# Performance work log

Hardware: AMD Instinct MI355X
Metric: run time of the kernel (lower is better)

## Reference

```python
import jax, jax.numpy as jnp
import numpy as np
import math

B, S, D = 16, 2048, 128
MASK_SENTINEL = -100

def setup_inputs() -> dict:
    key = jax.random.key(0)
    k1, k2, k3, k4 = jax.random.split(key, 4)
    value = jax.random.normal(k1, (B, S, D), dtype=jnp.float32)
    key_t = jax.random.normal(k2, (B, S, D), dtype=jnp.float32)
    query = jax.random.normal(k3, (B, S, D), dtype=jnp.float32)
    # mask uses -100 as the "masked out" sentinel, anything else is kept.
    bits = jax.random.randint(k4, (B, S, S), 0, 2, dtype=jnp.int32)
    mask = jnp.where(bits == 0, jnp.int32(MASK_SENTINEL), jnp.int32(0))
    return {"value": value, "key": key_t, "query": query, "mask": mask}

def reference(value, key, query, mask):
    # scores: [B, Sq, Sk]
    scale = 1.0 / math.sqrt(query.shape[-1])
    scores = jnp.einsum("bqd,bkd->bqk", query, key) * scale
    min_val = jnp.finfo(scores.dtype).min
    masked = jnp.where(mask == MASK_SENTINEL, min_val, scores)
    attn = jax.nn.softmax(masked, axis=-1)
    return jnp.einsum("bqk,bkd->bqd", attn, value)
```

## Files before the change

### kernel.cpp

```cpp
#include <hip/hip_runtime.h>
#include <hip/hip_bf16.h>

#define BATCH 16
#define SEQ   2048
#define DIM   128
#define QBLK  64
#define KVBLK 64
#define NT    (SEQ / KVBLK)
#define KPAD  136
#define VPAD  68
#define PPAD  72
#define L2E   1.4426950408889634f
#define THR   8.0f

typedef __attribute__((ext_vector_type(8))) short bf16x8;
typedef __attribute__((ext_vector_type(4))) short bf16x4;
typedef __attribute__((ext_vector_type(4))) float f32x4;

__device__ __forceinline__ short f2bf(float f) {
  union { float f; unsigned u; } v; v.f = f;
  unsigned r = (v.u + 0x7FFFu + ((v.u >> 16) & 1u)) >> 16;
  return (short)r;
}

__device__ __forceinline__ void issue_kv(const float* __restrict__ Kb,
                                         const float* __restrict__ Vb,
                                         int k0, int tid,
                                         float4 (&kreg)[8], float (&vreg)[32]) {
  #pragma unroll
  for (int it = 0; it < 8; ++it) {
    const int idx = tid + it * 256;
    kreg[it] = *(const float4*)(Kb + (size_t)(k0 + (idx >> 5)) * DIM + (idx & 31) * 4);
  }
  const int d = tid & 127;
  #pragma unroll
  for (int st = 0; st < 8; ++st) {
    const int kv0 = ((tid >> 7) + 2 * st) * 4;
    #pragma unroll
    for (int j = 0; j < 4; ++j)
      vreg[st * 4 + j] = Vb[(size_t)(k0 + kv0 + j) * DIM + d];
  }
}

__device__ __forceinline__ void issue_m(const int* const (&Mrow)[4], int k0,
                                        int (&mreg)[16]) {
  #pragma unroll
  for (int sub = 0; sub < 4; ++sub)
    #pragma unroll
    for (int i = 0; i < 4; ++i)
      mreg[sub * 4 + i] = Mrow[i][k0 + sub * 16];
}

__global__ __launch_bounds__(256, 2) void attn_fwd(
    const float* __restrict__ Vg, const float* __restrict__ Kg,
    const float* __restrict__ Qg, const int* __restrict__ Mg,
    float* __restrict__ Og) {
  __shared__ short lds_k[KVBLK * KPAD];
  __shared__ short lds_vt[DIM * VPAD];
  __shared__ short lds_p[4][16 * PPAD];

  const int tid = threadIdx.x;
  const int w   = tid >> 6;
  const int l   = tid & 63;
  const int g   = l >> 4;
  const int lr  = l & 15;

  const int blk = blockIdx.x;
  const int b   = blk >> 5;
  const int q0  = (blk & 31) * QBLK;

  const float scale = 0.08838834764831845f;

  bf16x8 qa[4];
  {
    const float* qbase = Qg + ((size_t)b * SEQ + (size_t)(q0 + w * 16 + lr)) * DIM + g * 8;
    #pragma unroll
    for (int kk = 0; kk < 4; ++kk) {
      const float4 x0 = *(const float4*)(qbase + kk * 32);
      const float4 x1 = *(const float4*)(qbase + kk * 32 + 4);
      bf16x8 f;
      f[0] = f2bf(x0.x * scale); f[1] = f2bf(x0.y * scale);
      f[2] = f2bf(x0.z * scale); f[3] = f2bf(x0.w * scale);
      f[4] = f2bf(x1.x * scale); f[5] = f2bf(x1.y * scale);
      f[6] = f2bf(x1.z * scale); f[7] = f2bf(x1.w * scale);
      qa[kk] = f;
    }
  }

  f32x4 acc[8];
  #pragma unroll
  for (int t = 0; t < 8; ++t) acc[t] = (f32x4){0.f, 0.f, 0.f, 0.f};
  float mrow[4] = {-1e30f, -1e30f, -1e30f, -1e30f};
  float lsum[4] = {0.f, 0.f, 0.f, 0.f};

  const float* Kb = Kg + (size_t)b * SEQ * DIM;
  const float* Vb = Vg + (size_t)b * SEQ * DIM;
  const int*   Mb = Mg + (size_t)b * SEQ * SEQ;
  const int* const Mrow[4] = {
    Mb + (size_t)(q0 + w * 16 + 4 * g + 0) * SEQ + lr,
    Mb + (size_t)(q0 + w * 16 + 4 * g + 1) * SEQ + lr,
    Mb + (size_t)(q0 + w * 16 + 4 * g + 2) * SEQ + lr,
    Mb + (size_t)(q0 + w * 16 + 4 * g + 3) * SEQ + lr };

  float4 kreg[8];
  float  vreg[32];
  int    mreg[16];

  issue_kv(Kb, Vb, 0, tid, kreg, vreg);
  issue_m(Mrow, 0, mreg);

  for (int t = 0; t < NT; ++t) {
    const int k0 = t * KVBLK;
    __syncthreads();

    #pragma unroll
    for (int it = 0; it < 8; ++it) {
      const int idx = tid + it * 256;
      const int row = idx >> 5;
      const int c4  = idx & 31;
      const float4 x = kreg[it];
      bf16x4 y;
      y[0] = f2bf(x.x); y[1] = f2bf(x.y); y[2] = f2bf(x.z); y[3] = f2bf(x.w);
      *(bf16x4*)&lds_k[row * KPAD + c4 * 4] = y;
    }
    {
      const int d = tid & 127;
      #pragma unroll
      for (int st = 0; st < 8; ++st) {
        const int kv0 = ((tid >> 7) + 2 * st) * 4;
        bf16x4 y;
        y[0] = f2bf(vreg[st * 4 + 0]); y[1] = f2bf(vreg[st * 4 + 1]);
        y[2] = f2bf(vreg[st * 4 + 2]); y[3] = f2bf(vreg[st * 4 + 3]);
        *(bf16x4*)&lds_vt[d * VPAD + kv0] = y;
      }
    }
    __syncthreads();

    if (t + 1 < NT) issue_kv(Kb, Vb, k0 + KVBLK, tid, kreg, vreg);

    f32x4 s[4];
    #pragma unroll
    for (int sub = 0; sub < 4; ++sub) {
      f32x4 sv = (f32x4){0.f, 0.f, 0.f, 0.f};
      const int krow = sub * 16 + lr;
      #pragma unroll
      for (int kk = 0; kk < 4; ++kk) {
        bf16x8 kb = *(const bf16x8*)&lds_k[krow * KPAD + kk * 32 + g * 8];
        sv = __builtin_amdgcn_mfma_f32_16x16x32_bf16(qa[kk], kb, sv, 0, 0, 0);
      }
      s[sub] = sv;
    }

    #pragma unroll
    for (int sub = 0; sub < 4; ++sub) {
      #pragma unroll
      for (int i = 0; i < 4; ++i) {
        if (mreg[sub * 4 + i] == -100) s[sub][i] = -1e30f;
      }
    }
    if (t + 1 < NT) issue_m(Mrow, k0 + KVBLK, mreg);

    float tmax[4];
    bool chg = false;
    #pragma unroll
    for (int i = 0; i < 4; ++i) {
      float tm = fmaxf(fmaxf(s[0][i], s[1][i]), fmaxf(s[2][i], s[3][i]));
      #pragma unroll
      for (int dlt = 1; dlt < 16; dlt <<= 1)
        tm = fmaxf(tm, __shfl_xor(tm, dlt, 16));
      tmax[i] = tm;
      chg = chg || (tm > mrow[i] + THR);
    }
    if (__any(chg)) {
      #pragma unroll
      for (int i = 0; i < 4; ++i) {
        const float mnew = fmaxf(mrow[i], tmax[i]);
        const float alpha = __builtin_amdgcn_exp2f((mrow[i] - mnew) * L2E);
        mrow[i] = mnew;
        lsum[i] *= alpha;
        #pragma unroll
        for (int t8 = 0; t8 < 8; ++t8) acc[t8][i] *= alpha;
      }
    }

    #pragma unroll
    for (int sub = 0; sub < 4; ++sub) {
      #pragma unroll
      for (int i = 0; i < 4; ++i) {
        const float p = __builtin_amdgcn_exp2f((s[sub][i] - mrow[i]) * L2E);
        lsum[i] += p;
        lds_p[w][(4 * g + i) * PPAD + sub * 16 + lr] = f2bf(p);
      }
    }

    bf16x8 pa[2];
    #pragma unroll
    for (int kk = 0; kk < 2; ++kk)
      pa[kk] = *(const bf16x8*)&lds_p[w][lr * PPAD + kk * 32 + g * 8];
    #pragma unroll
    for (int t8 = 0; t8 < 8; ++t8) {
      #pragma unroll
      for (int kk = 0; kk < 2; ++kk) {
        const int voff = (16 * t8 + lr) * VPAD + kk * 32 + g * 8;
        bf16x4 v0 = *(const bf16x4*)&lds_vt[voff];
        bf16x4 v1 = *(const bf16x4*)&lds_vt[voff + 4];
        bf16x8 vb = __builtin_shufflevector(v0, v1, 0, 1, 2, 3, 4, 5, 6, 7);
        acc[t8] = __builtin_amdgcn_mfma_f32_16x16x32_bf16(pa[kk], vb, acc[t8], 0, 0, 0);
      }
    }
  }

  float rden[4];
  #pragma unroll
  for (int i = 0; i < 4; ++i) {
    float sm = lsum[i];
    #pragma unroll
    for (int dlt = 1; dlt < 16; dlt <<= 1) sm += __shfl_xor(sm, dlt, 16);
    rden[i] = 1.f / sm;
  }
  float* ob = Og + ((size_t)b * SEQ + (size_t)(q0 + w * 16)) * DIM;
  #pragma unroll
  for (int t8 = 0; t8 < 8; ++t8) {
    #pragma unroll
    for (int i = 0; i < 4; ++i)
      ob[(4 * g + i) * DIM + 16 * t8 + lr] = acc[t8][i] * rden[i];
  }
}

extern "C" void kernel_launch(void* const* d_in, const int* in_sizes, int n_in,
                              void* d_out, int out_size, void* d_ws, size_t ws_size,
                              hipStream_t stream) {
  (void)in_sizes; (void)n_in; (void)d_ws; (void)ws_size; (void)out_size;
  const float* Vg = (const float*)d_in[0];
  const float* Kg = (const float*)d_in[1];
  const float* Qg = (const float*)d_in[2];
  const int*   Mg = (const int*)d_in[3];
  float* Og = (float*)d_out;
  dim3 grid(BATCH * (SEQ / QBLK));
  attn_fwd<<<grid, 256, 0, stream>>>(Vg, Kg, Qg, Mg, Og);
}
```

Baseline: 128.7 us.

## Pre-convert K and transposed V to bf16, split KV across waves per query tile

Two new pre-kernels convert K to bf16 and V to a transposed bf16 layout in workspace. The main kernel now gives each block 16 query rows and splits the KV range across its 4 waves, each loading K and V fragments straight from global memory without LDS staging. The per-wave partial softmax results are merged through LDS at the end, and blocks are swizzled for L2 locality. The intent is to drop the per-block fp32-to-bf16 conversion and LDS traffic and to raise occupancy and parallelism, at the cost of extra launches and a workspace dependency, with a fallback to the old kernel when the workspace is too small.

New measurement: 296.9 us. +130.7%, slower.

```diff
diff --git a/kernel.cpp b/kernel.cpp
--- a/kernel.cpp
+++ b/kernel.cpp
@@ -4,29 +4,253 @@
 #define BATCH 16
 #define SEQ   2048
 #define DIM   128
+#define L2E   1.4426950408889634f
+#define THR   8.0f
+#define MSENT -100
+
+typedef __attribute__((ext_vector_type(8))) short bf16x8;
+typedef __attribute__((ext_vector_type(4))) short bf16x4;
+typedef __attribute__((ext_vector_type(4))) float f32x4;
+typedef __attribute__((ext_vector_type(4))) int   i32x4;
+typedef __attribute__((ext_vector_type(2))) unsigned u32x2;
+typedef __attribute__((ext_vector_type(4))) unsigned u32x4;
+
+__device__ __forceinline__ unsigned short f2bf(float f) {
+  union { float f; unsigned u; } v; v.f = f;
+  return (unsigned short)((v.u + 0x7FFFu + ((v.u >> 16) & 1u)) >> 16);
+}
+__device__ __forceinline__ unsigned packbf(float a, float b) {
+  return ((unsigned)f2bf(b) << 16) | (unsigned)f2bf(a);
+}
+
+__global__ __launch_bounds__(256) void cvt_k(const float* __restrict__ K,
+                                             short* __restrict__ Kb) {
+  const size_t i = ((size_t)blockIdx.x * 256 + threadIdx.x) * 8;
+  f32x4 a = __builtin_nontemporal_load((const f32x4*)(K + i));
+  f32x4 b = __builtin_nontemporal_load((const f32x4*)(K + i + 4));
+  u32x4 o = { packbf(a[0], a[1]), packbf(a[2], a[3]),
+              packbf(b[0], b[1]), packbf(b[2], b[3]) };
+  *(u32x4*)(Kb + i) = o;
+}
+
+__global__ __launch_bounds__(256) void cvt_vt(const float* __restrict__ V,
+                                              short* __restrict__ Vt) {
+  __shared__ unsigned t32[64][65];
+  const int tid = threadIdx.x;
+  const int b  = blockIdx.x >> 5;
+  const int s0 = (blockIdx.x & 31) * 64;
+  #pragma unroll
+  for (int it = 0; it < 8; ++it) {
+    const int idx = tid + it * 256;
+    const int r = idx >> 5, c4 = idx & 31;
+    f32x4 x = __builtin_nontemporal_load(
+        (const f32x4*)(V + ((size_t)b * SEQ + s0 + r) * DIM + c4 * 4));
+    t32[r][c4 * 2]     = packbf(x[0], x[1]);
+    t32[r][c4 * 2 + 1] = packbf(x[2], x[3]);
+  }
+  __syncthreads();
+  const int d = tid >> 1, sh = tid & 1;
+  unsigned short outv[32];
+  #pragma unroll
+  for (int j = 0; j < 32; ++j) {
+    const unsigned u = t32[sh * 32 + j][d >> 1];
+    outv[j] = (d & 1) ? (unsigned short)(u >> 16) : (unsigned short)(u & 0xffff);
+  }
+  short* op = Vt + ((size_t)b * DIM + d) * SEQ + s0 + sh * 32;
+  #pragma unroll
+  for (int q = 0; q < 4; ++q) {
+    bf16x8 y;
+    #pragma unroll
+    for (int j = 0; j < 8; ++j) y[j] = (short)outv[q * 8 + j];
+    *(bf16x8*)(op + q * 8) = y;
+  }
+}
+
+__global__ __launch_bounds__(256, 3) void attn_split(
+    const float* __restrict__ Qg, const short* __restrict__ Kbf,
+    const short* __restrict__ Vt, const int* __restrict__ Mg,
+    float* __restrict__ Og) {
+  __shared__ unsigned pa_lds[4][16][40];
+  __shared__ float accw[4][16][132];
+  __shared__ float MW[4][16], LW[4][16];
+
+  const int tid = threadIdx.x;
+  const int w = tid >> 6, l = tid & 63, g = l >> 4, lr = l & 15;
+  const int bid = blockIdx.x;
+  const int swz = (bid & 7) * 256 + (bid >> 3);
+  const int b   = swz >> 7;
+  const int q0  = (swz & 127) * 16;
+  const int kvw = w * (SEQ / 4);
+
+  const float scale = 0.08838834764831845f;
+
+  bf16x8 qa[4];
+  {
+    const float* qbase = Qg + ((size_t)b * SEQ + q0 + lr) * DIM + g * 8;
+    #pragma unroll
+    for (int kk = 0; kk < 4; ++kk) {
+      f32x4 x0 = *(const f32x4*)(qbase + kk * 32);
+      f32x4 x1 = *(const f32x4*)(qbase + kk * 32 + 4);
+      bf16x8 f;
+      #pragma unroll
+      for (int j = 0; j < 4; ++j) {
+        f[j]     = (short)f2bf(x0[j] * scale);
+        f[j + 4] = (short)f2bf(x1[j] * scale);
+      }
+      qa[kk] = f;
+    }
+  }
+
+  const short* Kb = Kbf + (size_t)b * SEQ * DIM;
+  const short* Vb = Vt  + (size_t)b * DIM * SEQ;
+  const int*   Mr = Mg + (size_t)b * SEQ * SEQ + (size_t)(q0 + lr) * SEQ;
+
+  f32x4 acc[8];
+  #pragma unroll
+  for (int t = 0; t < 8; ++t) acc[t] = (f32x4){0.f, 0.f, 0.f, 0.f};
+  float mrow = -1e30f, lsum = 0.f;
+
+  i32x4 mreg[4];
+  #pragma unroll
+  for (int sub = 0; sub < 4; ++sub)
+    mreg[sub] = __builtin_nontemporal_load(
+        (const i32x4*)(Mr + kvw + 16 * sub + 4 * g));
+
+  for (int t = 0; t < 8; ++t) {
+    const int kv0 = kvw + t * 64;
+
+    f32x4 s[4];
+    #pragma unroll
+    for (int sub = 0; sub < 4; ++sub) s[sub] = (f32x4){0.f, 0.f, 0.f, 0.f};
+    #pragma unroll
+    for (int kk = 0; kk < 4; ++kk) {
+      bf16x8 kf0 = *(const bf16x8*)(Kb + (size_t)(kv0      + lr) * DIM + kk * 32 + g * 8);
+      bf16x8 kf1 = *(const bf16x8*)(Kb + (size_t)(kv0 + 16 + lr) * DIM + kk * 32 + g * 8);
+      bf16x8 kf2 = *(const bf16x8*)(Kb + (size_t)(kv0 + 32 + lr) * DIM + kk * 32 + g * 8);
+      bf16x8 kf3 = *(const bf16x8*)(Kb + (size_t)(kv0 + 48 + lr) * DIM + kk * 32 + g * 8);
+      s[0] = __builtin_amdgcn_mfma_f32_16x16x32_bf16(kf0, qa[kk], s[0], 0, 0, 0);
+      s[1] = __builtin_amdgcn_mfma_f32_16x16x32_bf16(kf1, qa[kk], s[1], 0, 0, 0);
+      s[2] = __builtin_amdgcn_mfma_f32_16x16x32_bf16(kf2, qa[kk], s[2], 0, 0, 0);
+      s[3] = __builtin_amdgcn_mfma_f32_16x16x32_bf16(kf3, qa[kk], s[3], 0, 0, 0);
+    }
+
+    bf16x8 vf[2][2];
+    #pragma unroll
+    for (int p = 0; p < 2; ++p)
+      #pragma unroll
+      for (int kk2 = 0; kk2 < 2; ++kk2)
+        vf[p][kk2] = *(const bf16x8*)(Vb + (size_t)(16 * p + lr) * SEQ +
+                                      kv0 + kk2 * 32 + g * 8);
+
+    #pragma unroll
+    for (int sub = 0; sub < 4; ++sub) {
+      #pragma unroll
+      for (int i = 0; i < 4; ++i)
+        if (mreg[sub][i] == MSENT) s[sub][i] = -1e30f;
+    }
+    if (t < 7) {
+      #pragma unroll
+      for (int sub = 0; sub < 4; ++sub)
+        mreg[sub] = __builtin_nontemporal_load(
+            (const i32x4*)(Mr + kv0 + 64 + 16 * sub + 4 * g));
+    }
+
+    float tm = s[0][0];
+    #pragma unroll
+    for (int sub = 0; sub < 4; ++sub)
+      #pragma unroll
+      for (int i = 0; i < 4; ++i) tm = fmaxf(tm, s[sub][i]);
+    tm = fmaxf(tm, __shfl_xor(tm, 16));
+    tm = fmaxf(tm, __shfl_xor(tm, 32));
+    if (__any(tm > mrow + THR)) {
+      const float mnew = fmaxf(mrow, tm);
+      const float al = __builtin_amdgcn_exp2f((mrow - mnew) * L2E);
+      mrow = mnew; lsum *= al;
+      float av[4];
+      #pragma unroll
+      for (int i = 0; i < 4; ++i) av[i] = __shfl(al, g * 16 + 4 * g + i);
+      #pragma unroll
+      for (int t8 = 0; t8 < 8; ++t8)
+        #pragma unroll
+        for (int i = 0; i < 4; ++i) acc[t8][i] *= av[i];
+    }
+
+    unsigned pk[4][2];
+    #pragma unroll
+    for (int sub = 0; sub < 4; ++sub) {
+      const float p0 = __builtin_amdgcn_exp2f((s[sub][0] - mrow) * L2E);
+      const float p1 = __builtin_amdgcn_exp2f((s[sub][1] - mrow) * L2E);
+      const float p2 = __builtin_amdgcn_exp2f((s[sub][2] - mrow) * L2E);
+      const float p3 = __builtin_amdgcn_exp2f((s[sub][3] - mrow) * L2E);
+      lsum += (p0 + p1) + (p2 + p3);
+      pk[sub][0] = packbf(p0, p1);
+      pk[sub][1] = packbf(p2, p3);
+    }
+    #pragma unroll
+    for (int sub = 0; sub < 4; ++sub)
+      *(u32x2*)&pa_lds[w][lr][8 * sub + 2 * g] = (u32x2){pk[sub][0], pk[sub][1]};
+    bf16x8 pa0 = *(const bf16x8*)&pa_lds[w][lr][4 * g];
+    bf16x8 pa1 = *(const bf16x8*)&pa_lds[w][lr][16 + 4 * g];
+
+    #pragma unroll
+    for (int t8 = 0; t8 < 8; ++t8) {
+      const int cur = t8 & 1;
+      acc[t8] = __builtin_amdgcn_mfma_f32_16x16x32_bf16(pa0, vf[cur][0], acc[t8], 0, 0, 0);
+      acc[t8] = __builtin_amdgcn_mfma_f32_16x16x32_bf16(pa1, vf[cur][1], acc[t8], 0, 0, 0);
+      if (t8 < 6) {
+        #pragma unroll
+        for (int kk2 = 0; kk2 < 2; ++kk2)
+          vf[cur][kk2] = *(const bf16x8*)(Vb + (size_t)(16 * (t8 + 2) + lr) * SEQ +
+                                          kv0 + kk2 * 32 + g * 8);
+      }
+    }
+  }
+
+  lsum += __shfl_xor(lsum, 16);
+  lsum += __shfl_xor(lsum, 32);
+  if (l < 16) { MW[w][l] = mrow; LW[w][l] = lsum; }
+  #pragma unroll
+  for (int t8 = 0; t8 < 8; ++t8)
+    #pragma unroll
+    for (int i = 0; i < 4; ++i)
+      accw[w][4 * g + i][16 * t8 + lr] = acc[t8][i];
+  __syncthreads();
+
+  const int r = tid >> 4, db = (tid & 15) * 8;
+  const float m0 = MW[0][r], m1 = MW[1][r], m2 = MW[2][r], m3 = MW[3][r];
+  const float M = fmaxf(fmaxf(m0, m1), fmaxf(m2, m3));
+  const float sc0 = __builtin_amdgcn_exp2f((m0 - M) * L2E);
+  const float sc1 = __builtin_amdgcn_exp2f((m1 - M) * L2E);
+  const float sc2 = __builtin_amdgcn_exp2f((m2 - M) * L2E);
+  const float sc3 = __builtin_amdgcn_exp2f((m3 - M) * L2E);
+  const float L = sc0 * LW[0][r] + sc1 * LW[1][r] + sc2 * LW[2][r] + sc3 * LW[3][r];
+  const float inv = 1.f / L;
+  f32x4 oa = (f32x4){0.f, 0.f, 0.f, 0.f}, ob = (f32x4){0.f, 0.f, 0.f, 0.f};
+  const float scv[4] = {sc0, sc1, sc2, sc3};
+  #pragma unroll
+  for (int w4 = 0; w4 < 4; ++w4) {
+    f32x4 x0 = *(const f32x4*)&accw[w4][r][db];
+    f32x4 x1 = *(const f32x4*)&accw[w4][r][db + 4];
+    oa += scv[w4] * x0;
+    ob += scv[w4] * x1;
+  }
+  oa *= inv; ob *= inv;
+  float* op = Og + ((size_t)b * SEQ + q0 + r) * DIM + db;
+  __builtin_nontemporal_store(oa, (f32x4*)op);
+  __builtin_nontemporal_store(ob, (f32x4*)(op + 4));
+}
+
 #define QBLK  64
 #define KVBLK 64
 #define NT    (SEQ / KVBLK)
 #define KPAD  136
 #define VPAD  68
 #define PPAD  72
-#define L2E   1.4426950408889634f
-#define THR   8.0f
-
-typedef __attribute__((ext_vector_type(8))) short bf16x8;
-typedef __attribute__((ext_vector_type(4))) short bf16x4;
-typedef __attribute__((ext_vector_type(4))) float f32x4;
-
-__device__ __forceinline__ short f2bf(float f) {
-  union { float f; unsigned u; } v; v.f = f;
-  unsigned r = (v.u + 0x7FFFu + ((v.u >> 16) & 1u)) >> 16;
-  return (short)r;
-}
-
-__device__ __forceinline__ void issue_kv(const float* __restrict__ Kb,
-                                         const float* __restrict__ Vb,
-                                         int k0, int tid,
-                                         float4 (&kreg)[8], float (&vreg)[32]) {
+
+__device__ __forceinline__ void issue_kv_fb(const float* __restrict__ Kb,
+                                            const float* __restrict__ Vb,
+                                            int k0, int tid,
+                                            float4 (&kreg)[8], float (&vreg)[32]) {
   #pragma unroll
   for (int it = 0; it < 8; ++it) {
     const int idx = tid + it * 256;
@@ -41,9 +265,8 @@
       vreg[st * 4 + j] = Vb[(size_t)(k0 + kv0 + j) * DIM + d];
   }
 }
-
-__device__ __forceinline__ void issue_m(const int* const (&Mrow)[4], int k0,
-                                        int (&mreg)[16]) {
+__device__ __forceinline__ void issue_m_fb(const int* const (&Mrow)[4], int k0,
+                                           int (&mreg)[16]) {
   #pragma unroll
   for (int sub = 0; sub < 4; ++sub)
     #pragma unroll
@@ -51,26 +274,17 @@
       mreg[sub * 4 + i] = Mrow[i][k0 + sub * 16];
 }
 
-__global__ __launch_bounds__(256, 2) void attn_fwd(
+__global__ __launch_bounds__(256, 2) void attn_fwd_fb(
     const float* __restrict__ Vg, const float* __restrict__ Kg,
     const float* __restrict__ Qg, const int* __restrict__ Mg,
     float* __restrict__ Og) {
   __shared__ short lds_k[KVBLK * KPAD];
   __shared__ short lds_vt[DIM * VPAD];
   __shared__ short lds_p[4][16 * PPAD];
-
   const int tid = threadIdx.x;
-  const int w   = tid >> 6;
-  const int l   = tid & 63;
-  const int g   = l >> 4;
-  const int lr  = l & 15;
-
-  const int blk = blockIdx.x;
-  const int b   = blk >> 5;
-  const int q0  = (blk & 31) * QBLK;
-
+  const int w = tid >> 6, l = tid & 63, g = l >> 4, lr = l & 15;
+  const int blk = blockIdx.x, b = blk >> 5, q0 = (blk & 31) * QBLK;
   const float scale = 0.08838834764831845f;
-
   bf16x8 qa[4];
   {
     const float* qbase = Qg + ((size_t)b * SEQ + (size_t)(q0 + w * 16 + lr)) * DIM + g * 8;
@@ -79,20 +293,18 @@
       const float4 x0 = *(const float4*)(qbase + kk * 32);
       const float4 x1 = *(const float4*)(qbase + kk * 32 + 4);
       bf16x8 f;
-      f[0] = f2bf(x0.x * scale); f[1] = f2bf(x0.y * scale);
-      f[2] = f2bf(x0.z * scale); f[3] = f2bf(x0.w * scale);
-      f[4] = f2bf(x1.x * scale); f[5] = f2bf(x1.y * scale);
-      f[6] = f2bf(x1.z * scale); f[7] = f2bf(x1.w * scale);
+      f[0] = (short)f2bf(x0.x * scale); f[1] = (short)f2bf(x0.y * scale);
+      f[2] = (short)f2bf(x0.z * scale); f[3] = (short)f2bf(x0.w * scale);
+      f[4] = (short)f2bf(x1.x * scale); f[5] = (short)f2bf(x1.y * scale);
+      f[6] = (short)f2bf(x1.z * scale); f[7] = (short)f2bf(x1.w * scale);
       qa[kk] = f;
     }
   }
-
   f32x4 acc[8];
   #pragma unroll
   for (int t = 0; t < 8; ++t) acc[t] = (f32x4){0.f, 0.f, 0.f, 0.f};
   float mrow[4] = {-1e30f, -1e30f, -1e30f, -1e30f};
   float lsum[4] = {0.f, 0.f, 0.f, 0.f};
-
   const float* Kb = Kg + (size_t)b * SEQ * DIM;
   const float* Vb = Vg + (size_t)b * SEQ * DIM;
   const int*   Mb = Mg + (size_t)b * SEQ * SEQ;
@@ -101,26 +313,20 @@
     Mb + (size_t)(q0 + w * 16 + 4 * g + 1) * SEQ + lr,
     Mb + (size_t)(q0 + w * 16 + 4 * g + 2) * SEQ + lr,
     Mb + (size_t)(q0 + w * 16 + 4 * g + 3) * SEQ + lr };
-
-  float4 kreg[8];
-  float  vreg[32];
-  int    mreg[16];
-
-  issue_kv(Kb, Vb, 0, tid, kreg, vreg);
-  issue_m(Mrow, 0, mreg);
-
+  float4 kreg[8]; float vreg[32]; int mreg[16];
+  issue_kv_fb(Kb, Vb, 0, tid, kreg, vreg);
+  issue_m_fb(Mrow, 0, mreg);
   for (int t = 0; t < NT; ++t) {
     const int k0 = t * KVBLK;
     __syncthreads();
-
     #pragma unroll
     for (int it = 0; it < 8; ++it) {
       const int idx = tid + it * 256;
-      const int row = idx >> 5;
-      const int c4  = idx & 31;
+      const int row = idx >> 5, c4 = idx & 31;
       const float4 x = kreg[it];
       bf16x4 y;
-      y[0] = f2bf(x.x); y[1] = f2bf(x.y); y[2] = f2bf(x.z); y[3] = f2bf(x.w);
+      y[0] = (short)f2bf(x.x); y[1] = (short)f2bf(x.y);
+      y[2] = (short)f2bf(x.z); y[3] = (short)f2bf(x.w);
       *(bf16x4*)&lds_k[row * KPAD + c4 * 4] = y;
     }
     {
@@ -129,15 +335,13 @@
       for (int st = 0; st < 8; ++st) {
         const int kv0 = ((tid >> 7) + 2 * st) * 4;
         bf16x4 y;
-        y[0] = f2bf(vreg[st * 4 + 0]); y[1] = f2bf(vreg[st * 4 + 1]);
-        y[2] = f2bf(vreg[st * 4 + 2]); y[3] = f2bf(vreg[st * 4 + 3]);
+        y[0] = (short)f2bf(vreg[st * 4 + 0]); y[1] = (short)f2bf(vreg[st * 4 + 1]);
+        y[2] = (short)f2bf(vreg[st * 4 + 2]); y[3] = (short)f2bf(vreg[st * 4 + 3]);
         *(bf16x4*)&lds_vt[d * VPAD + kv0] = y;
       }
     }
     __syncthreads();
-
-    if (t + 1 < NT) issue_kv(Kb, Vb, k0 + KVBLK, tid, kreg, vreg);
-
+    if (t + 1 < NT) issue_kv_fb(Kb, Vb, k0 + KVBLK, tid, kreg, vreg);
     f32x4 s[4];
     #pragma unroll
     for (int sub = 0; sub < 4; ++sub) {
@@ -150,18 +354,13 @@
       }
       s[sub] = sv;
     }
-
-    #pragma unroll
-    for (int sub = 0; sub < 4; ++sub) {
-      #pragma unroll
-      for (int i = 0; i < 4; ++i) {
-        if (mreg[sub * 4 + i] == -100) s[sub][i] = -1e30f;
-      }
-    }
-    if (t + 1 < NT) issue_m(Mrow, k0 + KVBLK, mreg);
-
-    float tmax[4];
-    bool chg = false;
+    #pragma unroll
+    for (int sub = 0; sub < 4; ++sub)
+      #pragma unroll
+      for (int i = 0; i < 4; ++i)
+        if (mreg[sub * 4 + i] == MSENT) s[sub][i] = -1e30f;
+    if (t + 1 < NT) issue_m_fb(Mrow, k0 + KVBLK, mreg);
+    float tmax[4]; bool chg = false;
     #pragma unroll
     for (int i = 0; i < 4; ++i) {
       float tm = fmaxf(fmaxf(s[0][i], s[1][i]), fmaxf(s[2][i], s[3][i]));
@@ -176,29 +375,25 @@
       for (int i = 0; i < 4; ++i) {
         const float mnew = fmaxf(mrow[i], tmax[i]);
         const float alpha = __builtin_amdgcn_exp2f((mrow[i] - mnew) * L2E);
-        mrow[i] = mnew;
-        lsum[i] *= alpha;
+        mrow[i] = mnew; lsum[i] *= alpha;
         #pragma unroll
         for (int t8 = 0; t8 < 8; ++t8) acc[t8][i] *= alpha;
       }
     }
-
-    #pragma unroll
-    for (int sub = 0; sub < 4; ++sub) {
+    #pragma unroll
+    for (int sub = 0; sub < 4; ++sub)
       #pragma unroll
       for (int i = 0; i < 4; ++i) {
         const float p = __builtin_amdgcn_exp2f((s[sub][i] - mrow[i]) * L2E);
         lsum[i] += p;
-        lds_p[w][(4 * g + i) * PPAD + sub * 16 + lr] = f2bf(p);
-      }
-    }
-
+        lds_p[w][(4 * g + i) * PPAD + sub * 16 + lr] = (short)f2bf(p);
+      }
     bf16x8 pa[2];
     #pragma unroll
     for (int kk = 0; kk < 2; ++kk)
       pa[kk] = *(const bf16x8*)&lds_p[w][lr * PPAD + kk * 32 + g * 8];
     #pragma unroll
-    for (int t8 = 0; t8 < 8; ++t8) {
+    for (int t8 = 0; t8 < 8; ++t8)
       #pragma unroll
       for (int kk = 0; kk < 2; ++kk) {
         const int voff = (16 * t8 + lr) * VPAD + kk * 32 + g * 8;
@@ -207,9 +402,7 @@
         bf16x8 vb = __builtin_shufflevector(v0, v1, 0, 1, 2, 3, 4, 5, 6, 7);
         acc[t8] = __builtin_amdgcn_mfma_f32_16x16x32_bf16(pa[kk], vb, acc[t8], 0, 0, 0);
       }
-    }
-  }
-
+  }
   float rden[4];
   #pragma unroll
   for (int i = 0; i < 4; ++i) {
@@ -220,22 +413,30 @@
   }
   float* ob = Og + ((size_t)b * SEQ + (size_t)(q0 + w * 16)) * DIM;
   #pragma unroll
-  for (int t8 = 0; t8 < 8; ++t8) {
+  for (int t8 = 0; t8 < 8; ++t8)
     #pragma unroll
     for (int i = 0; i < 4; ++i)
       ob[(4 * g + i) * DIM + 16 * t8 + lr] = acc[t8][i] * rden[i];
-  }
 }
 
 extern "C" void kernel_launch(void* const* d_in, const int* in_sizes, int n_in,
                               void* d_out, int out_size, void* d_ws, size_t ws_size,
                               hipStream_t stream) {
-  (void)in_sizes; (void)n_in; (void)d_ws; (void)ws_size; (void)out_size;
+  (void)in_sizes; (void)n_in; (void)out_size;
   const float* Vg = (const float*)d_in[0];
   const float* Kg = (const float*)d_in[1];
   const float* Qg = (const float*)d_in[2];
   const int*   Mg = (const int*)d_in[3];
   float* Og = (float*)d_out;
-  dim3 grid(BATCH * (SEQ / QBLK));
-  attn_fwd<<<grid, 256, 0, stream>>>(Vg, Kg, Qg, Mg, Og);
-}
+
+  const size_t need = (size_t)2 * BATCH * SEQ * DIM * sizeof(short);
+  if (ws_size >= need) {
+    short* Kbf = (short*)d_ws;
+    short* Vt  = Kbf + (size_t)BATCH * SEQ * DIM;
+    cvt_k<<<dim3(BATCH * SEQ * DIM / (8 * 256)), 256, 0, stream>>>(Kg, Kbf);
+    cvt_vt<<<dim3(BATCH * (SEQ / 64)), 256, 0, stream>>>(Vg, Vt);
+    attn_split<<<dim3(BATCH * (SEQ / 16)), 256, 0, stream>>>(Qg, Kbf, Vt, Mg, Og);
+  } else {
+    attn_fwd_fb<<<dim3(BATCH * (SEQ / QBLK)), 256, 0, stream>>>(Vg, Kg, Qg, Mg, Og);
+  }
+}
```

## Pre-convert K and transposed V to bf16 and stream via async LDS loads

Applied to the files above, without the earlier changes.

Two small pre-pass kernels convert K to bf16 and V to a transposed bf16 layout in the workspace, so the attention kernel no longer redoes fp32 loads and conversion for every query block. The main loop now double-buffers K/V tiles in LDS using global_load_lds with an XOR swizzle, overlapping the next tile's fetch with compute and needing one barrier per iteration. Mask loads become nontemporal. This adds two extra launches, needs workspace memory, and doubles LDS use, which may lower occupancy.

After: 118.4 us. 8.0% less time.

```diff
diff --git a/kernel.cpp b/kernel.cpp
--- a/kernel.cpp
+++ b/kernel.cpp
@@ -7,56 +7,99 @@
 #define QBLK  64
 #define KVBLK 64
 #define NT    (SEQ / KVBLK)
-#define KPAD  136
-#define VPAD  68
 #define PPAD  72
 #define L2E   1.4426950408889634f
 #define THR   8.0f
+#define MSENT -100
 
 typedef __attribute__((ext_vector_type(8))) short bf16x8;
 typedef __attribute__((ext_vector_type(4))) short bf16x4;
 typedef __attribute__((ext_vector_type(4))) float f32x4;
-
-__device__ __forceinline__ short f2bf(float f) {
+typedef __attribute__((ext_vector_type(4))) unsigned u32x4;
+
+__device__ __forceinline__ unsigned short f2bf(float f) {
   union { float f; unsigned u; } v; v.f = f;
-  unsigned r = (v.u + 0x7FFFu + ((v.u >> 16) & 1u)) >> 16;
-  return (short)r;
-}
-
-__device__ __forceinline__ void issue_kv(const float* __restrict__ Kb,
-                                         const float* __restrict__ Vb,
-                                         int k0, int tid,
-                                         float4 (&kreg)[8], float (&vreg)[32]) {
+  return (unsigned short)((v.u + 0x7FFFu + ((v.u >> 16) & 1u)) >> 16);
+}
+__device__ __forceinline__ unsigned packbf(float a, float b) {
+  return ((unsigned)f2bf(b) << 16) | (unsigned)f2bf(a);
+}
+
+__global__ __launch_bounds__(256) void cvt_k(const float* __restrict__ K,
+                                             short* __restrict__ Kb) {
+  const size_t i = ((size_t)blockIdx.x * 256 + threadIdx.x) * 8;
+  f32x4 a = __builtin_nontemporal_load((const f32x4*)(K + i));
+  f32x4 b = __builtin_nontemporal_load((const f32x4*)(K + i + 4));
+  u32x4 o = { packbf(a[0], a[1]), packbf(a[2], a[3]),
+              packbf(b[0], b[1]), packbf(b[2], b[3]) };
+  *(u32x4*)(Kb + i) = o;
+}
+
+__global__ __launch_bounds__(256) void cvt_vt(const float* __restrict__ V,
+                                              short* __restrict__ Vt) {
+  __shared__ unsigned t32[64][65];
+  const int tid = threadIdx.x;
+  const int b  = blockIdx.x >> 5;
+  const int s0 = (blockIdx.x & 31) * 64;
   #pragma unroll
   for (int it = 0; it < 8; ++it) {
     const int idx = tid + it * 256;
-    kreg[it] = *(const float4*)(Kb + (size_t)(k0 + (idx >> 5)) * DIM + (idx & 31) * 4);
-  }
-  const int d = tid & 127;
-  #pragma unroll
-  for (int st = 0; st < 8; ++st) {
-    const int kv0 = ((tid >> 7) + 2 * st) * 4;
-    #pragma unroll
-    for (int j = 0; j < 4; ++j)
-      vreg[st * 4 + j] = Vb[(size_t)(k0 + kv0 + j) * DIM + d];
-  }
-}
-
-__device__ __forceinline__ void issue_m(const int* const (&Mrow)[4], int k0,
-                                        int (&mreg)[16]) {
-  #pragma unroll
-  for (int sub = 0; sub < 4; ++sub)
-    #pragma unroll
-    for (int i = 0; i < 4; ++i)
-      mreg[sub * 4 + i] = Mrow[i][k0 + sub * 16];
+    const int r = idx >> 5, c4 = idx & 31;
+    f32x4 x = __builtin_nontemporal_load(
+        (const f32x4*)(V + ((size_t)b * SEQ + s0 + r) * DIM + c4 * 4));
+    t32[r][c4 * 2]     = packbf(x[0], x[1]);
+    t32[r][c4 * 2 + 1] = packbf(x[2], x[3]);
+  }
+  __syncthreads();
+  const int d = tid >> 1, sh = tid & 1;
+  unsigned short outv[32];
+  #pragma unroll
+  for (int j = 0; j < 32; ++j) {
+    const unsigned u = t32[sh * 32 + j][d >> 1];
+    outv[j] = (d & 1) ? (unsigned short)(u >> 16) : (unsigned short)(u & 0xffff);
+  }
+  short* op = Vt + ((size_t)b * DIM + d) * SEQ + s0 + sh * 32;
+  #pragma unroll
+  for (int q = 0; q < 4; ++q) {
+    bf16x8 y;
+    #pragma unroll
+    for (int j = 0; j < 8; ++j) y[j] = (short)outv[q * 8 + j];
+    *(bf16x8*)(op + q * 8) = y;
+  }
+}
+
+__device__ __forceinline__ void gload16(const void* g, void* l) {
+  __builtin_amdgcn_global_load_lds(
+      (const __attribute__((address_space(1))) unsigned*)g,
+      (__attribute__((address_space(3))) unsigned*)l, 16, 0, 0);
+}
+
+__device__ __forceinline__ void stage_kv(const char* __restrict__ Kb2,
+                                         const char* __restrict__ Vtb2,
+                                         int k0, int w, int l,
+                                         short* kbuf, short* vbuf) {
+  #pragma unroll
+  for (int it = 0; it < 4; ++it) {
+    const int ch = w * 4 + it;
+    const int r  = ch * 4 + (l >> 4);
+    const int cs = ((l & 15) * 16) ^ ((r & 7) << 4);
+    gload16(Kb2 + (size_t)(k0 + r) * 256 + cs, (char*)kbuf + ch * 1024);
+  }
+  #pragma unroll
+  for (int it = 0; it < 4; ++it) {
+    const int ch = w * 4 + it;
+    const int d  = ch * 8 + (l >> 3);
+    const int cs = ((l & 7) * 16) ^ ((d & 7) << 4);
+    gload16(Vtb2 + (size_t)d * (SEQ * 2) + k0 * 2 + cs, (char*)vbuf + ch * 1024);
+  }
 }
 
 __global__ __launch_bounds__(256, 2) void attn_fwd(
-    const float* __restrict__ Vg, const float* __restrict__ Kg,
+    const short* __restrict__ Kbf, const short* __restrict__ Vt,
     const float* __restrict__ Qg, const int* __restrict__ Mg,
     float* __restrict__ Og) {
-  __shared__ short lds_k[KVBLK * KPAD];
-  __shared__ short lds_vt[DIM * VPAD];
+  __shared__ short lds_k[2][KVBLK * DIM];
+  __shared__ short lds_v[2][DIM * KVBLK];
   __shared__ short lds_p[4][16 * PPAD];
 
   const int tid = threadIdx.x;
@@ -71,72 +114,56 @@
 
   const float scale = 0.08838834764831845f;
 
-  bf16x8 qa[4];
-  {
-    const float* qbase = Qg + ((size_t)b * SEQ + (size_t)(q0 + w * 16 + lr)) * DIM + g * 8;
-    #pragma unroll
-    for (int kk = 0; kk < 4; ++kk) {
-      const float4 x0 = *(const float4*)(qbase + kk * 32);
-      const float4 x1 = *(const float4*)(qbase + kk * 32 + 4);
-      bf16x8 f;
-      f[0] = f2bf(x0.x * scale); f[1] = f2bf(x0.y * scale);
-      f[2] = f2bf(x0.z * scale); f[3] = f2bf(x0.w * scale);
-      f[4] = f2bf(x1.x * scale); f[5] = f2bf(x1.y * scale);
-      f[6] = f2bf(x1.z * scale); f[7] = f2bf(x1.w * scale);
-      qa[kk] = f;
-    }
-  }
-
-  f32x4 acc[8];
-  #pragma unroll
-  for (int t = 0; t < 8; ++t) acc[t] = (f32x4){0.f, 0.f, 0.f, 0.f};
-  float mrow[4] = {-1e30f, -1e30f, -1e30f, -1e30f};
-  float lsum[4] = {0.f, 0.f, 0.f, 0.f};
-
-  const float* Kb = Kg + (size_t)b * SEQ * DIM;
-  const float* Vb = Vg + (size_t)b * SEQ * DIM;
-  const int*   Mb = Mg + (size_t)b * SEQ * SEQ;
+  const char* Kb2  = (const char*)(Kbf + (size_t)b * SEQ * DIM);
+  const char* Vtb2 = (const char*)(Vt  + (size_t)b * DIM * SEQ);
+  const int*  Mb   = Mg + (size_t)b * SEQ * SEQ;
   const int* const Mrow[4] = {
     Mb + (size_t)(q0 + w * 16 + 4 * g + 0) * SEQ + lr,
     Mb + (size_t)(q0 + w * 16 + 4 * g + 1) * SEQ + lr,
     Mb + (size_t)(q0 + w * 16 + 4 * g + 2) * SEQ + lr,
     Mb + (size_t)(q0 + w * 16 + 4 * g + 3) * SEQ + lr };
 
-  float4 kreg[8];
-  float  vreg[32];
-  int    mreg[16];
-
-  issue_kv(Kb, Vb, 0, tid, kreg, vreg);
-  issue_m(Mrow, 0, mreg);
+  stage_kv(Kb2, Vtb2, 0, w, l, lds_k[0], lds_v[0]);
+  int mreg[16];
+  #pragma unroll
+  for (int sub = 0; sub < 4; ++sub)
+    #pragma unroll
+    for (int i = 0; i < 4; ++i)
+      mreg[sub * 4 + i] = __builtin_nontemporal_load(Mrow[i] + sub * 16);
+
+  bf16x8 qa[4];
+  {
+    const float* qbase = Qg + ((size_t)b * SEQ + (size_t)(q0 + w * 16 + lr)) * DIM + g * 8;
+    #pragma unroll
+    for (int kk = 0; kk < 4; ++kk) {
+      f32x4 x0 = *(const f32x4*)(qbase + kk * 32);
+      f32x4 x1 = *(const f32x4*)(qbase + kk * 32 + 4);
+      bf16x8 f;
+      #pragma unroll
+      for (int j = 0; j < 4; ++j) {
+        f[j]     = (short)f2bf(x0[j] * scale);
+        f[j + 4] = (short)f2bf(x1[j] * scale);
+      }
+      qa[kk] = f;
+    }
+  }
+
+  f32x4 acc[8];
+  #pragma unroll
+  for (int t = 0; t < 8; ++t) acc[t] = (f32x4){0.f, 0.f, 0.f, 0.f};
+  float mrow[4] = {-1e30f, -1e30f, -1e30f, -1e30f};
+  float lsum[4] = {0.f, 0.f, 0.f, 0.f};
+
+  __syncthreads();
+  int cur = 0;
 
   for (int t = 0; t < NT; ++t) {
     const int k0 = t * KVBLK;
-    __syncthreads();
-
-    #pragma unroll
-    for (int it = 0; it < 8; ++it) {
-      const int idx = tid + it * 256;
-      const int row = idx >> 5;
-      const int c4  = idx & 31;
-      const float4 x = kreg[it];
-      bf16x4 y;
-      y[0] = f2bf(x.x); y[1] = f2bf(x.y); y[2] = f2bf(x.z); y[3] = f2bf(x.w);
-      *(bf16x4*)&lds_k[row * KPAD + c4 * 4] = y;
-    }
-    {
-      const int d = tid & 127;
-      #pragma unroll
-      for (int st = 0; st < 8; ++st) {
-        const int kv0 = ((tid >> 7) + 2 * st) * 4;
-        bf16x4 y;
-        y[0] = f2bf(vreg[st * 4 + 0]); y[1] = f2bf(vreg[st * 4 + 1]);
-        y[2] = f2bf(vreg[st * 4 + 2]); y[3] = f2bf(vreg[st * 4 + 3]);
-        *(bf16x4*)&lds_vt[d * VPAD + kv0] = y;
-      }
-    }
-    __syncthreads();
-
-    if (t + 1 < NT) issue_kv(Kb, Vb, k0 + KVBLK, tid, kreg, vreg);
+    if (t + 1 < NT)
+      stage_kv(Kb2, Vtb2, k0 + KVBLK, w, l, lds_k[cur ^ 1], lds_v[cur ^ 1]);
+
+    const char* kbuf = (const char*)lds_k[cur];
+    const char* vbuf = (const char*)lds_v[cur];
 
     f32x4 s[4];
     #pragma unroll
@@ -145,20 +172,26 @@
       const int krow = sub * 16 + lr;
       #pragma unroll
       for (int kk = 0; kk < 4; ++kk) {
-        bf16x8 kb = *(const bf16x8*)&lds_k[krow * KPAD + kk * 32 + g * 8];
+        const int cb = (kk * 64 + g * 16) ^ ((krow & 7) << 4);
+        bf16x8 kb = *(const bf16x8*)(kbuf + krow * 256 + cb);
         sv = __builtin_amdgcn_mfma_f32_16x16x32_bf16(qa[kk], kb, sv, 0, 0, 0);
       }
       s[sub] = sv;
     }
 
     #pragma unroll
-    for (int sub = 0; sub < 4; ++sub) {
-      #pragma unroll
-      for (int i = 0; i < 4; ++i) {
-        if (mreg[sub * 4 + i] == -100) s[sub][i] = -1e30f;
-      }
-    }
-    if (t + 1 < NT) issue_m(Mrow, k0 + KVBLK, mreg);
+    for (int sub = 0; sub < 4; ++sub)
+      #pragma unroll
+      for (int i = 0; i < 4; ++i)
+        if (mreg[sub * 4 + i] == MSENT) s[sub][i] = -1e30f;
+    if (t + 1 < NT) {
+      #pragma unroll
+      for (int sub = 0; sub < 4; ++sub)
+        #pragma unroll
+        for (int i = 0; i < 4; ++i)
+          mreg[sub * 4 + i] =
+              __builtin_nontemporal_load(Mrow[i] + k0 + KVBLK + sub * 16);
+    }
 
     float tmax[4];
     bool chg = false;
@@ -184,14 +217,13 @@
     }
 
     #pragma unroll
-    for (int sub = 0; sub < 4; ++sub) {
+    for (int sub = 0; sub < 4; ++sub)
       #pragma unroll
       for (int i = 0; i < 4; ++i) {
         const float p = __builtin_amdgcn_exp2f((s[sub][i] - mrow[i]) * L2E);
         lsum[i] += p;
-        lds_p[w][(4 * g + i) * PPAD + sub * 16 + lr] = f2bf(p);
-      }
-    }
+        lds_p[w][(4 * g + i) * PPAD + sub * 16 + lr] = (short)f2bf(p);
+      }
 
     bf16x8 pa[2];
     #pragma unroll
@@ -199,15 +231,17 @@
       pa[kk] = *(const bf16x8*)&lds_p[w][lr * PPAD + kk * 32 + g * 8];
     #pragma unroll
     for (int t8 = 0; t8 < 8; ++t8) {
+      const int d = 16 * t8 + lr;
       #pragma unroll
       for (int kk = 0; kk < 2; ++kk) {
-        const int voff = (16 * t8 + lr) * VPAD + kk * 32 + g * 8;
-        bf16x4 v0 = *(const bf16x4*)&lds_vt[voff];
-        bf16x4 v1 = *(const bf16x4*)&lds_vt[voff + 4];
-        bf16x8 vb = __builtin_shufflevector(v0, v1, 0, 1, 2, 3, 4, 5, 6, 7);
+        const int cb = (kk * 64 + g * 16) ^ ((d & 7) << 4);
+        bf16x8 vb = *(const bf16x8*)(vbuf + d * 128 + cb);
         acc[t8] = __builtin_amdgcn_mfma_f32_16x16x32_bf16(pa[kk], vb, acc[t8], 0, 0, 0);
       }
     }
+
+    __syncthreads();
+    cur ^= 1;
   }
 
   float rden[4];
@@ -220,22 +254,25 @@
   }
   float* ob = Og + ((size_t)b * SEQ + (size_t)(q0 + w * 16)) * DIM;
   #pragma unroll
-  for (int t8 = 0; t8 < 8; ++t8) {
+  for (int t8 = 0; t8 < 8; ++t8)
     #pragma unroll
     for (int i = 0; i < 4; ++i)
       ob[(4 * g + i) * DIM + 16 * t8 + lr] = acc[t8][i] * rden[i];
-  }
 }
 
 extern "C" void kernel_launch(void* const* d_in, const int* in_sizes, int n_in,
                               void* d_out, int out_size, void* d_ws, size_t ws_size,
                               hipStream_t stream) {
-  (void)in_sizes; (void)n_in; (void)d_ws; (void)ws_size; (void)out_size;
+  (void)in_sizes; (void)n_in; (void)out_size; (void)ws_size;
   const float* Vg = (const float*)d_in[0];
   const float* Kg = (const float*)d_in[1];
   const float* Qg = (const float*)d_in[2];
   const int*   Mg = (const int*)d_in[3];
   float* Og = (float*)d_out;
-  dim3 grid(BATCH * (SEQ / QBLK));
-  attn_fwd<<<grid, 256, 0, stream>>>(Vg, Kg, Qg, Mg, Og);
-}
+
+  short* Kbf = (short*)d_ws;
+  short* Vt  = Kbf + (size_t)BATCH * SEQ * DIM;
+  cvt_k<<<dim3(BATCH * SEQ * DIM / (8 * 256)), 256, 0, stream>>>(Kg, Kbf);
+  cvt_vt<<<dim3(BATCH * (SEQ / 64)), 256, 0, stream>>>(Vg, Vt);
+  attn_fwd<<<dim3(BATCH * (SEQ / QBLK)), 256, 0, stream>>>(Kbf, Vt, Qg, Mg, Og);
+}
```
